# Performance work log

Measured on AMD Instinct MI355X. Metric: run time of the kernel, lower is better.

## Reference

```python
import jax, jax.numpy as jnp
import numpy as np

DIM = 2048
N_HEADS = 16
HEAD_DIM = DIM // N_HEADS
ROPE_THETA = 10000.0


def setup_inputs() -> dict:
    key = jax.random.key(0)
    k1, k2, k3 = jax.random.split(key, 3)
    B, T = 2, 2048
    x = jax.random.normal(k1, (B, T, DIM), dtype=jnp.float32)
    # nn.Linear weight layout: [out_features, in_features]; scale like torch init
    w_qkv = jax.random.normal(k2, (3 * DIM, DIM), dtype=jnp.float32) / jnp.sqrt(DIM)
    w_out = jax.random.normal(k3, (DIM, DIM), dtype=jnp.float32) / jnp.sqrt(DIM)
    return {"x": x, "w_qkv": w_qkv, "w_out": w_out}


def _rope_cos_sin(T, start_pos=0, dtype=jnp.float32):
    inv_freq = 1.0 / (ROPE_THETA ** (jnp.arange(0, HEAD_DIM, 2, dtype=jnp.float32) / HEAD_DIM))
    pos = jnp.arange(start_pos, start_pos + T, dtype=jnp.float32)
    ang = pos[:, None] * inv_freq[None, :]           # [T, HEAD_DIM//2]
    return jnp.cos(ang).astype(dtype), jnp.sin(ang).astype(dtype)


def _apply_rope(t, cos, sin):
    # t: [B, T, H, D]; rotate-half convention
    t1, t2 = jnp.split(t, 2, axis=-1)
    cos = cos[None, :, None, :]
    sin = sin[None, :, None, :]
    return jnp.concatenate([t1 * cos - t2 * sin, t1 * sin + t2 * cos], axis=-1)


def reference(x, w_qkv, w_out):
    B, T, C = x.shape
    qkv = jnp.einsum('btc,oc->bto', x, w_qkv)        # [B, T, 3C]
    q, k, v = jnp.split(qkv, 3, axis=-1)
    q = q.reshape(B, T, N_HEADS, HEAD_DIM)
    k = k.reshape(B, T, N_HEADS, HEAD_DIM)
    v = v.reshape(B, T, N_HEADS, HEAD_DIM)
    cos, sin = _rope_cos_sin(T, 0, x.dtype)
    q = _apply_rope(q, cos, sin)
    k = _apply_rope(k, cos, sin)
    scale = 1.0 / np.sqrt(HEAD_DIM)
    att = jnp.einsum('bqhd,bkhd->bhqk', q, k) * scale  # [B, H, T, T]
    causal = jnp.tril(jnp.ones((T, T), dtype=bool))
    att = jnp.where(causal[None, None], att, jnp.finfo(att.dtype).min)
    att = jax.nn.softmax(att, axis=-1)
    out = jnp.einsum('bhqk,bkhd->bqhd', att, v).reshape(B, T, C)
    return jnp.einsum('btc,oc->bto', out, w_out)
```

## Files before the change

kernel.cpp:

```cpp
#include <hip/hip_runtime.h>
#include <hip/hip_bf16.h>
#include <cmath>
#include <type_traits>

#define DIMC 2048
#define NHEADS 16
#define HDIM 128
#define SEQT 2048
#define BATCH 2

using frag8 = __attribute__((ext_vector_type(8))) short;
using f32x4 = __attribute__((ext_vector_type(4))) float;

#define MFMA(a, b, c) __builtin_amdgcn_mfma_f32_16x16x32_bf16((a), (b), (c), 0, 0, 0)

#define GLOAD_LDS(g, l)                                              \
  __builtin_amdgcn_global_load_lds(                                  \
      (const __attribute__((address_space(1))) void*)(g),            \
      (__attribute__((address_space(3))) void*)(l), 16, 0, 0)

__global__ void zero_out_kernel(float* __restrict__ out, int n) {
  int i = blockIdx.x * blockDim.x + threadIdx.x;
  if (i < n) out[i] = 0.0f;
}

__global__ void cast_f32_bf16(const float* __restrict__ in,
                              __hip_bfloat16* __restrict__ out, int n4) {
  int i = blockIdx.x * blockDim.x + threadIdx.x;
  if (i >= n4) return;
  float4 v = reinterpret_cast<const float4*>(in)[i];
  union { __hip_bfloat16 h[4]; ushort4 u; } cv;
  cv.h[0] = __float2bfloat16(v.x);
  cv.h[1] = __float2bfloat16(v.y);
  cv.h[2] = __float2bfloat16(v.z);
  cv.h[3] = __float2bfloat16(v.w);
  reinterpret_cast<ushort4*>(out)[i] = cv.u;
}

__global__ void rope_tab_kernel(float* __restrict__ tab) {
  int idx = blockIdx.x * blockDim.x + threadIdx.x;
  if (idx >= SEQT * 64) return;
  int j = idx & 63, t = idx >> 6;
  float inv = expf(-9.210340371976184f * (float)j / 64.0f);
  float ang = (float)t * inv;
  tab[idx * 2] = cosf(ang);
  tab[idx * 2 + 1] = sinf(ang);
}

template <typename CT>
__global__ __launch_bounds__(256) void gemm_bt(
    const __hip_bfloat16* __restrict__ A, const __hip_bfloat16* __restrict__ Bm,
    CT* __restrict__ C, int M, int N, int K) {
  __shared__ __hip_bfloat16 As[128 * 32];
  __shared__ __hip_bfloat16 Bs[128 * 32];
  const int tid = threadIdx.x;
  const int lane = tid & 63;
  const int wave = tid >> 6;
  const int wr = wave >> 1, wc = wave & 1;
  const int m0 = blockIdx.y * 128, n0 = blockIdx.x * 128;
  const int lr = lane & 15, lg = lane >> 4;

  const __hip_bfloat16* Ap = A + (size_t)(m0 + (tid >> 2)) * K + (tid & 3) * 8;
  const __hip_bfloat16* Bp = Bm + (size_t)(n0 + (tid >> 2)) * K + (tid & 3) * 8;
  __hip_bfloat16* Asd = As + tid * 8;
  __hip_bfloat16* Bsd = Bs + tid * 8;

  f32x4 acc[4][4] = {};

  for (int k0 = 0; k0 < K; k0 += 32) {
    GLOAD_LDS(Ap + k0, Asd);
    GLOAD_LDS(Ap + (size_t)64 * K + k0, Asd + 2048);
    GLOAD_LDS(Bp + k0, Bsd);
    GLOAD_LDS(Bp + (size_t)64 * K + k0, Bsd + 2048);
    __syncthreads();
    frag8 a[4], b[4];
#pragma unroll
    for (int mi = 0; mi < 4; ++mi)
      a[mi] = *reinterpret_cast<const frag8*>(&As[(wr * 64 + mi * 16 + lr) * 32 + lg * 8]);
#pragma unroll
    for (int nj = 0; nj < 4; ++nj)
      b[nj] = *reinterpret_cast<const frag8*>(&Bs[(wc * 64 + nj * 16 + lr) * 32 + lg * 8]);
#pragma unroll
    for (int mi = 0; mi < 4; ++mi)
#pragma unroll
      for (int nj = 0; nj < 4; ++nj)
        acc[mi][nj] = MFMA(a[mi], b[nj], acc[mi][nj]);
    __syncthreads();
  }

#pragma unroll
  for (int mi = 0; mi < 4; ++mi)
#pragma unroll
    for (int nj = 0; nj < 4; ++nj)
#pragma unroll
      for (int i = 0; i < 4; ++i) {
        int row = m0 + wr * 64 + mi * 16 + lg * 4 + i;
        int col = n0 + wc * 64 + nj * 16 + lr;
        float v = acc[mi][nj][i];
        if constexpr (std::is_same<CT, __hip_bfloat16>::value)
          C[(size_t)row * N + col] = __float2bfloat16(v);
        else
          C[(size_t)row * N + col] = v;
      }
}

__global__ void rope_qk(const __hip_bfloat16* __restrict__ qkv,
                        const float* __restrict__ tab,
                        __hip_bfloat16* __restrict__ q,
                        __hip_bfloat16* __restrict__ k) {
  int idx = blockIdx.x * blockDim.x + threadIdx.x;
  if (idx >= BATCH * SEQT * NHEADS * 64) return;
  int j = idx & 63;
  int h = (idx >> 6) & 15;
  int t = (idx >> 10) & 2047;
  int b = idx >> 21;
  float c = tab[(t * 64 + j) * 2];
  float s = tab[(t * 64 + j) * 2 + 1];
  size_t qi = (size_t)(b * SEQT + t) * (3 * DIMC) + h * HDIM + j;
  float q1 = __bfloat162float(qkv[qi]);
  float q2 = __bfloat162float(qkv[qi + 64]);
  float k1 = __bfloat162float(qkv[qi + DIMC]);
  float k2 = __bfloat162float(qkv[qi + DIMC + 64]);
  const float sc = 0.08838834764831845f;
  size_t oi = ((size_t)(b * NHEADS + h) * SEQT + t) * HDIM + j;
  q[oi] = __float2bfloat16((q1 * c - q2 * s) * sc);
  q[oi + 64] = __float2bfloat16((q1 * s + q2 * c) * sc);
  k[oi] = __float2bfloat16(k1 * c - k2 * s);
  k[oi + 64] = __float2bfloat16(k1 * s + k2 * c);
}

__global__ __launch_bounds__(256) void transpose_v(
    const __hip_bfloat16* __restrict__ qkv, __hip_bfloat16* __restrict__ vt) {
  __shared__ __hip_bfloat16 tile[32][33];
  int t0 = blockIdx.x * 32;
  int d0 = blockIdx.y * 32;
  int bh = blockIdx.z;
  int b = bh >> 4, h = bh & 15;
  int x = threadIdx.x & 31, y = threadIdx.x >> 5;
#pragma unroll
  for (int r = 0; r < 4; ++r) {
    int tr = r * 8 + y;
    tile[tr][x] = qkv[(size_t)(b * SEQT + t0 + tr) * (3 * DIMC) + 2 * DIMC + h * HDIM + d0 + x];
  }
  __syncthreads();
#pragma unroll
  for (int r = 0; r < 4; ++r) {
    int dr = r * 8 + y;
    vt[((size_t)bh * HDIM + d0 + dr) * SEQT + t0 + x] = tile[x][dr];
  }
}

__global__ __launch_bounds__(64) void flash_attn(
    const __hip_bfloat16* __restrict__ q, const __hip_bfloat16* __restrict__ k,
    const __hip_bfloat16* __restrict__ vt, __hip_bfloat16* __restrict__ ctx) {
  const int qt = 63 - (blockIdx.x >> 5);
  const int bh = blockIdx.x & 31;
  const int lane = threadIdx.x;
  const int lr = lane & 15, lg = lane >> 4;
  const size_t base = (size_t)bh * SEQT * HDIM;

  __shared__ __hip_bfloat16 P[32 * 40];

  frag8 aq[2][4];
#pragma unroll
  for (int rt = 0; rt < 2; ++rt)
#pragma unroll
    for (int dc = 0; dc < 4; ++dc)
      aq[rt][dc] = *reinterpret_cast<const frag8*>(
          &q[base + (size_t)(qt * 32 + rt * 16 + lr) * HDIM + dc * 32 + lg * 8]);

  f32x4 o[2][8] = {};
  float mrun[2][4], lrun[2][4];
#pragma unroll
  for (int rt = 0; rt < 2; ++rt)
#pragma unroll
    for (int i = 0; i < 4; ++i) { mrun[rt][i] = -INFINITY; lrun[rt][i] = 0.f; }

  auto loadK = [&](frag8 (&bk)[2][4], int kb) {
#pragma unroll
    for (int st = 0; st < 2; ++st)
#pragma unroll
      for (int dc = 0; dc < 4; ++dc)
        bk[st][dc] = *reinterpret_cast<const frag8*>(
            &k[base + (size_t)(kb * 32 + st * 16 + lr) * HDIM + dc * 32 + lg * 8]);
  };
  auto loadV = [&](frag8 (&bv)[8], int kb) {
#pragma unroll
    for (int dt = 0; dt < 8; ++dt)
      bv[dt] = *reinterpret_cast<const frag8*>(
          &vt[base + (size_t)(dt * 16 + lr) * SEQT + kb * 32 + lg * 8]);
  };

  auto compute = [&](frag8 (&bk)[2][4], frag8 (&bv)[8], int kb) {
    f32x4 s[2][2] = {};
    __builtin_amdgcn_s_setprio(1);
#pragma unroll
    for (int rt = 0; rt < 2; ++rt)
#pragma unroll
      for (int st = 0; st < 2; ++st)
#pragma unroll
        for (int dc = 0; dc < 4; ++dc)
          s[rt][st] = MFMA(aq[rt][dc], bk[st][dc], s[rt][st]);
    __builtin_amdgcn_s_setprio(0);

    if (kb == qt) {
#pragma unroll
      for (int rt = 0; rt < 2; ++rt)
#pragma unroll
        for (int st = 0; st < 2; ++st)
#pragma unroll
          for (int i = 0; i < 4; ++i)
            if (st * 16 + lr > rt * 16 + lg * 4 + i) s[rt][st][i] = -INFINITY;
    }

#pragma unroll
    for (int rt = 0; rt < 2; ++rt)
#pragma unroll
      for (int i = 0; i < 4; ++i) {
        float pm = fmaxf(s[rt][0][i], s[rt][1][i]);
        pm = fmaxf(pm, __shfl_xor(pm, 1, 16));
        pm = fmaxf(pm, __shfl_xor(pm, 2, 16));
        pm = fmaxf(pm, __shfl_xor(pm, 4, 16));
        pm = fmaxf(pm, __shfl_xor(pm, 8, 16));
        float mn = fmaxf(mrun[rt][i], pm);
        float sf = __expf(mrun[rt][i] - mn);
        mrun[rt][i] = mn;
        float p0 = __expf(s[rt][0][i] - mn);
        float p1 = __expf(s[rt][1][i] - mn);
        float rs = p0 + p1;
        rs += __shfl_xor(rs, 1, 16);
        rs += __shfl_xor(rs, 2, 16);
        rs += __shfl_xor(rs, 4, 16);
        rs += __shfl_xor(rs, 8, 16);
        lrun[rt][i] = lrun[rt][i] * sf + rs;
#pragma unroll
        for (int dt = 0; dt < 8; ++dt) o[rt][dt][i] *= sf;
        P[(rt * 16 + lg * 4 + i) * 40 + lr] = __float2bfloat16(p0);
        P[(rt * 16 + lg * 4 + i) * 40 + 16 + lr] = __float2bfloat16(p1);
      }

    frag8 pa[2];
#pragma unroll
    for (int rt = 0; rt < 2; ++rt)
      pa[rt] = *reinterpret_cast<const frag8*>(&P[(rt * 16 + lr) * 40 + lg * 8]);

    __builtin_amdgcn_s_setprio(1);
#pragma unroll
    for (int rt = 0; rt < 2; ++rt)
#pragma unroll
      for (int dt = 0; dt < 8; ++dt)
        o[rt][dt] = MFMA(pa[rt], bv[dt], o[rt][dt]);
    __builtin_amdgcn_s_setprio(0);
  };

  frag8 kA[2][4], vA[8], kB[2][4], vB[8];
  loadK(kA, 0);
  loadV(vA, 0);
  int kb = 0;
  while (true) {
    if (kb + 1 <= qt) { loadK(kB, kb + 1); loadV(vB, kb + 1); }
    compute(kA, vA, kb);
    if (++kb > qt) break;
    if (kb + 1 <= qt) { loadK(kA, kb + 1); loadV(vA, kb + 1); }
    compute(kB, vB, kb);
    if (++kb > qt) break;
  }

  const int b = bh >> 4, h = bh & 15;
#pragma unroll
  for (int rt = 0; rt < 2; ++rt)
#pragma unroll
    for (int i = 0; i < 4; ++i) {
      float inv = 1.0f / lrun[rt][i];
      int row = qt * 32 + rt * 16 + lg * 4 + i;
#pragma unroll
      for (int dt = 0; dt < 8; ++dt)
        ctx[(size_t)(b * SEQT + row) * DIMC + h * HDIM + dt * 16 + lr] =
            __float2bfloat16(o[rt][dt][i] * inv);
    }
}

extern "C" void kernel_launch(void* const* d_in, const int* in_sizes, int n_in,
                              void* d_out, int out_size, void* d_ws, size_t ws_size,
                              hipStream_t stream) {
  const float* x = (const float*)d_in[0];
  const float* w_qkv = (const float*)d_in[1];
  const float* w_out = (const float*)d_in[2];
  float* out = (float*)d_out;
  char* ws = (char*)d_ws;

  const size_t WS_NEEDED = 110100480;
  if (ws_size < WS_NEEDED) {
    zero_out_kernel<<<(out_size + 255) / 256, 256, 0, stream>>>(out, out_size);
    return;
  }

  __hip_bfloat16* qkvb  = (__hip_bfloat16*)(ws);
  __hip_bfloat16* ctx   = (__hip_bfloat16*)(ws);
  __hip_bfloat16* qbuf  = (__hip_bfloat16*)(ws + 50331648);
  __hip_bfloat16* kbuf  = (__hip_bfloat16*)(ws + 67108864);
  __hip_bfloat16* vtb   = (__hip_bfloat16*)(ws + 83886080);
  __hip_bfloat16* xb    = (__hip_bfloat16*)(ws + 50331648);
  __hip_bfloat16* wqkvb = (__hip_bfloat16*)(ws + 67108864);
  __hip_bfloat16* woutb = (__hip_bfloat16*)(ws + 100663296);
  float* tab            = (float*)(ws + 109051904);

  cast_f32_bf16<<<8192, 256, 0, stream>>>(x, xb, 2097152);
  cast_f32_bf16<<<12288, 256, 0, stream>>>(w_qkv, wqkvb, 3145728);
  cast_f32_bf16<<<4096, 256, 0, stream>>>(w_out, woutb, 1048576);
  rope_tab_kernel<<<512, 256, 0, stream>>>(tab);
  gemm_bt<__hip_bfloat16><<<dim3(48, 32), 256, 0, stream>>>(xb, wqkvb, qkvb, 4096, 6144, 2048);
  rope_qk<<<16384, 256, 0, stream>>>(qkvb, tab, qbuf, kbuf);
  transpose_v<<<dim3(64, 4, 32), 256, 0, stream>>>(qkvb, vtb);
  flash_attn<<<2048, 64, 0, stream>>>(qbuf, kbuf, vtb, ctx);
  gemm_bt<float><<<dim3(16, 32), 256, 0, stream>>>(ctx, woutb, out, 4096, 2048, 2048);
}
```

Baseline: 529.7 us.

## Use exp2 softmax with lazy rescaling and deferred row-sum reduction

Folds log2(e) into the query scale so the attention softmax uses exp2 directly. Adds a threshold-based fast path that skips the running-max shuffle reduction and output rescaling when new scores don't exceed the running max by much. Row sums are kept per lane and reduced across lanes only once at the end. This cuts shuffle and VALU work per key block, at the cost of unnormalized P values above 1 in bf16 and a wave-uniform branch.

```diff
diff --git a/kernel.cpp b/kernel.cpp
--- a/kernel.cpp
+++ b/kernel.cpp
@@ -8,6 +8,8 @@
 #define HDIM 128
 #define SEQT 2048
 #define BATCH 2
+
+#define EXP2(x) __builtin_amdgcn_exp2f(x)
 
 using frag8 = __attribute__((ext_vector_type(8))) short;
 using f32x4 = __attribute__((ext_vector_type(4))) float;
@@ -121,7 +123,7 @@
   float q2 = __bfloat162float(qkv[qi + 64]);
   float k1 = __bfloat162float(qkv[qi + DIMC]);
   float k2 = __bfloat162float(qkv[qi + DIMC + 64]);
-  const float sc = 0.08838834764831845f;
+  const float sc = 0.12751744945137108f;
   size_t oi = ((size_t)(b * NHEADS + h) * SEQT + t) * HDIM + j;
   q[oi] = __float2bfloat16((q1 * c - q2 * s) * sc);
   q[oi + 64] = __float2bfloat16((q1 * s + q2 * c) * sc);
@@ -158,6 +160,7 @@
   const int lane = threadIdx.x;
   const int lr = lane & 15, lg = lane >> 4;
   const size_t base = (size_t)bh * SEQT * HDIM;
+  const float THR = 11.54f;
 
   __shared__ __hip_bfloat16 P[32 * 40];
 
@@ -213,31 +216,47 @@
             if (st * 16 + lr > rt * 16 + lg * 4 + i) s[rt][st][i] = -INFINITY;
     }
 
+    float excess = -INFINITY;
 #pragma unroll
     for (int rt = 0; rt < 2; ++rt)
 #pragma unroll
-      for (int i = 0; i < 4; ++i) {
-        float pm = fmaxf(s[rt][0][i], s[rt][1][i]);
-        pm = fmaxf(pm, __shfl_xor(pm, 1, 16));
-        pm = fmaxf(pm, __shfl_xor(pm, 2, 16));
-        pm = fmaxf(pm, __shfl_xor(pm, 4, 16));
-        pm = fmaxf(pm, __shfl_xor(pm, 8, 16));
-        float mn = fmaxf(mrun[rt][i], pm);
-        float sf = __expf(mrun[rt][i] - mn);
-        mrun[rt][i] = mn;
-        float p0 = __expf(s[rt][0][i] - mn);
-        float p1 = __expf(s[rt][1][i] - mn);
-        float rs = p0 + p1;
-        rs += __shfl_xor(rs, 1, 16);
-        rs += __shfl_xor(rs, 2, 16);
-        rs += __shfl_xor(rs, 4, 16);
-        rs += __shfl_xor(rs, 8, 16);
-        lrun[rt][i] = lrun[rt][i] * sf + rs;
-#pragma unroll
-        for (int dt = 0; dt < 8; ++dt) o[rt][dt][i] *= sf;
-        P[(rt * 16 + lg * 4 + i) * 40 + lr] = __float2bfloat16(p0);
-        P[(rt * 16 + lg * 4 + i) * 40 + 16 + lr] = __float2bfloat16(p1);
-      }
+      for (int i = 0; i < 4; ++i)
+        excess = fmaxf(excess,
+                       fmaxf(s[rt][0][i], s[rt][1][i]) - mrun[rt][i]);
+
+    if (__all(excess <= THR)) {
+#pragma unroll
+      for (int rt = 0; rt < 2; ++rt)
+#pragma unroll
+        for (int i = 0; i < 4; ++i) {
+          float p0 = EXP2(s[rt][0][i] - mrun[rt][i]);
+          float p1 = EXP2(s[rt][1][i] - mrun[rt][i]);
+          lrun[rt][i] += p0 + p1;
+          P[(rt * 16 + lg * 4 + i) * 40 + lr] = __float2bfloat16(p0);
+          P[(rt * 16 + lg * 4 + i) * 40 + 16 + lr] = __float2bfloat16(p1);
+        }
+    } else {
+#pragma unroll
+      for (int rt = 0; rt < 2; ++rt)
+#pragma unroll
+        for (int i = 0; i < 4; ++i) {
+          float pm = fmaxf(s[rt][0][i], s[rt][1][i]);
+          pm = fmaxf(pm, __shfl_xor(pm, 1, 16));
+          pm = fmaxf(pm, __shfl_xor(pm, 2, 16));
+          pm = fmaxf(pm, __shfl_xor(pm, 4, 16));
+          pm = fmaxf(pm, __shfl_xor(pm, 8, 16));
+          float mn = fmaxf(mrun[rt][i], pm);
+          float sf = EXP2(mrun[rt][i] - mn);
+          mrun[rt][i] = mn;
+          float p0 = EXP2(s[rt][0][i] - mn);
+          float p1 = EXP2(s[rt][1][i] - mn);
+          lrun[rt][i] = lrun[rt][i] * sf + (p0 + p1);
+#pragma unroll
+          for (int dt = 0; dt < 8; ++dt) o[rt][dt][i] *= sf;
+          P[(rt * 16 + lg * 4 + i) * 40 + lr] = __float2bfloat16(p0);
+          P[(rt * 16 + lg * 4 + i) * 40 + 16 + lr] = __float2bfloat16(p1);
+        }
+    }
 
     frag8 pa[2];
 #pragma unroll
@@ -271,7 +290,12 @@
   for (int rt = 0; rt < 2; ++rt)
 #pragma unroll
     for (int i = 0; i < 4; ++i) {
-      float inv = 1.0f / lrun[rt][i];
+      float ls = lrun[rt][i];
+      ls += __shfl_xor(ls, 1, 16);
+      ls += __shfl_xor(ls, 2, 16);
+      ls += __shfl_xor(ls, 4, 16);
+      ls += __shfl_xor(ls, 8, 16);
+      float inv = 1.0f / ls;
       int row = qt * 32 + rt * 16 + lg * 4 + i;
 #pragma unroll
       for (int dt = 0; dt < 8; ++dt)
```

Result: faster. 464.7 us (-12.3%).
